# Performance work log

Measured on AMD Instinct MI355X. Metric: run time of the kernel, lower is better.

## Reference

```python
import jax, jax.numpy as jnp
import numpy as np
import math

NUM_HEADS = 32
NUM_KV = 8
D = 128          # num_hidden == per-head dim in this module
S = 2048
B = 1
DK = 128
ROPE_BASE = 10000.0


def rope(x):
    # x: [B, H, S, D]; standard Llama-style RoPE (split-halves rotation) over positions.
    d = x.shape[-1]
    half = d // 2
    pos = jnp.arange(x.shape[2], dtype=jnp.float32)                       # [S]
    inv_freq = 1.0 / (ROPE_BASE ** (jnp.arange(half, dtype=jnp.float32) / half))
    ang = pos[:, None] * inv_freq[None, :]                                # [S, half]
    cos = jnp.cos(ang)
    sin = jnp.sin(ang)
    x1 = x[..., :half]
    x2 = x[..., half:]
    return jnp.concatenate([x1 * cos - x2 * sin, x1 * sin + x2 * cos], axis=-1)


def setup_inputs() -> dict:
    key = jax.random.key(0)
    ks = jax.random.split(key, 8)
    query = jax.random.normal(ks[0], (B, S, D), dtype=jnp.float32)
    k_in = jax.random.normal(ks[1], (B, S, D), dtype=jnp.float32)
    v_in = jax.random.normal(ks[2], (B, S, D), dtype=jnp.float32)
    # causal mask: 1 where attention allowed (lower triangle incl diagonal)
    mask = jnp.tril(jnp.ones((S, S), dtype=jnp.int32))[None, None]        # [1,1,S,S]
    sc = 0.02
    Wq = jax.random.normal(ks[3], (NUM_HEADS * D, D), dtype=jnp.float32) * sc
    bq = jnp.zeros((NUM_HEADS * D,), dtype=jnp.float32)
    Wk = jax.random.normal(ks[4], (NUM_KV * D, D), dtype=jnp.float32) * sc
    bk = jnp.zeros((NUM_KV * D,), dtype=jnp.float32)
    Wv = jax.random.normal(ks[5], (NUM_KV * D, D), dtype=jnp.float32) * sc
    bv = jnp.zeros((NUM_KV * D,), dtype=jnp.float32)
    Wo = jax.random.normal(ks[6], (D, NUM_HEADS * D), dtype=jnp.float32) * sc
    bo = jnp.zeros((D,), dtype=jnp.float32)
    return {"query": query, "key": k_in, "values": v_in, "mask": mask,
            "Wq": Wq, "bq": bq, "Wk": Wk, "bk": bk, "Wv": Wv, "bv": bv,
            "Wo": Wo, "bo": bo}


def reference(query, key, values, mask, Wq, bq, Wk, bk, Wv, bv, Wo, bo):
    Bq, Sq, Dh = query.shape
    # projections; torch Linear: x @ W.T + b. Note: view (reshape), not transpose,
    # exactly as in the original module.
    q = (query @ Wq.T + bq).reshape(Bq, NUM_HEADS, Sq, Dh)   # [B,H,S,D]
    k = (key @ Wk.T + bk).reshape(Bq, NUM_KV, Sq, Dh)        # [B,Hkv,S,D]
    v = (values @ Wv.T + bv).reshape(Bq, NUM_KV, Sq, Dh)
    rk = rope(k)
    rv = rope(v)  # module applies RoPE to values too (faithful)
    rep = NUM_HEADS // NUM_KV
    # torch .repeat((1, rep, 1, 1)) tiles whole head blocks -> jnp.tile
    rk = jnp.tile(rk, (1, rep, 1, 1))                        # [B,H,S,D]
    rv = jnp.tile(rv, (1, rep, 1, 1))
    scores = jnp.einsum('bhqd,bhkd->bhqk', q, rk) / math.sqrt(DK)
    scores = jnp.where(mask == 0, -jnp.inf, scores)
    attn = jax.nn.softmax(scores, axis=-1)
    out = jnp.einsum('bhqk,bhkd->bhqd', attn, rv)            # [B,H,S,D]
    out = out.transpose(0, 2, 1, 3).reshape(Bq, Sq, NUM_HEADS * Dh)
    return out @ Wo.T + bo
```

## Files before the change

### kernel.cpp

```cpp
#include <hip/hip_runtime.h>

typedef unsigned short u16;
typedef unsigned int u32;
typedef short frag_t __attribute__((ext_vector_type(8)));
typedef float f32x4 __attribute__((ext_vector_type(4)));

#define S_LEN 2048

__device__ __forceinline__ float bf2f(u32 u) {
  union { u32 i; float f; } v; v.i = u << 16; return v.f;
}
__device__ __forceinline__ u16 f2bf(float f) {
  u32 x = __float_as_uint(f);
  u32 r = (x + 0x7fffu + ((x >> 16) & 1u)) >> 16;
  return (u16)r;
}
__device__ __forceinline__ void unpack8(uint4 r, float* o) {
  o[0] = bf2f(r.x & 0xffffu); o[1] = bf2f(r.x >> 16);
  o[2] = bf2f(r.y & 0xffffu); o[3] = bf2f(r.y >> 16);
  o[4] = bf2f(r.z & 0xffffu); o[5] = bf2f(r.z >> 16);
  o[6] = bf2f(r.w & 0xffffu); o[7] = bf2f(r.w >> 16);
}
__device__ __forceinline__ u16 ld_in(const void* p, size_t idx, bool fp32) {
  if (fp32) return f2bf(((const float*)p)[idx]);
  return ((const u16*)p)[idx];
}
__device__ __forceinline__ uint4 ld8(const void* p, size_t eidx, bool fp32) {
  if (!fp32) return *(const uint4*)((const u16*)p + eidx);
  const float4* f = (const float4*)((const float*)p + eidx);
  float4 x = f[0], y = f[1];
  uint4 r;
  r.x = (u32)f2bf(x.x) | ((u32)f2bf(x.y) << 16);
  r.y = (u32)f2bf(x.z) | ((u32)f2bf(x.w) << 16);
  r.z = (u32)f2bf(y.x) | ((u32)f2bf(y.y) << 16);
  r.w = (u32)f2bf(y.z) | ((u32)f2bf(y.w) << 16);
  return r;
}

__global__ __launch_bounds__(256) void proj_all(
    const void* __restrict__ query, const void* __restrict__ key,
    const void* __restrict__ values,
    const void* __restrict__ Wq, const void* __restrict__ bq,
    const void* __restrict__ Wk, const void* __restrict__ bk,
    const void* __restrict__ Wv, const void* __restrict__ bv,
    u16* __restrict__ Qb, u16* __restrict__ Kb, u16* __restrict__ Vtmp,
    u32* __restrict__ flag_out) {
  __shared__ u16 As[128][136];
  __shared__ u16 Ws[128][136];
  __shared__ u32 flagS;
  u16 (*Cs)[136] = As;
  const int t = threadIdx.x;
  if (t < 64) {
    u32 e = ((u32)((const u16*)query)[2 * t] >> 7) & 0xFFu;
    bool ok = (e >= 110u && e <= 140u);
    unsigned long long b = __ballot(ok);
    if (t == 0) flagS = (__popcll(b) < 32) ? 1u : 0u;
  }
  __syncthreads();
  const bool fp32 = (flagS != 0u);
  if (t == 0 && blockIdx.x == 0 && blockIdx.y == 0) *flag_out = flagS;
  const int x = blockIdx.x;
  const void *A, *W, *bias;
  u16* C; int N, n0;
  if (x < 32)      { A = query;  W = Wq; bias = bq; C = Qb;   N = 4096; n0 = x << 7; }
  else if (x < 40) { A = key;    W = Wk; bias = bk; C = Kb;   N = 1024; n0 = (x - 32) << 7; }
  else             { A = values; W = Wv; bias = bv; C = Vtmp; N = 1024; n0 = (x - 40) << 7; }
  const float osc = (x < 32) ? 0.12751743f : 1.0f;
  const int m0 = blockIdx.y << 7;
#pragma unroll
  for (int i = 0; i < 8; ++i) {
    int task = t + (i << 8);
    int row = task >> 4, ch = (task & 15) << 3;
    *(uint4*)&As[row][ch] = ld8(A, (size_t)(m0 + row) * 128 + ch, fp32);
    *(uint4*)&Ws[row][ch] = ld8(W, (size_t)(n0 + row) * 128 + ch, fp32);
  }
  __syncthreads();
  const int lane = t & 63, w = t >> 6, quad = lane >> 4, l15 = lane & 15;
  const int rm = (w & 1) << 6, rn = (w >> 1) << 6;
  f32x4 acc[4][4];
#pragma unroll
  for (int mt = 0; mt < 4; ++mt)
#pragma unroll
    for (int nt = 0; nt < 4; ++nt) acc[mt][nt] = 0.f;
#pragma unroll
  for (int mtp = 0; mtp < 2; ++mtp) {
    frag_t a0[4], a1[4];
#pragma unroll
    for (int kc = 0; kc < 4; ++kc) {
      a0[kc] = *(const frag_t*)&As[rm + mtp * 32 + l15][kc * 32 + quad * 8];
      a1[kc] = *(const frag_t*)&As[rm + mtp * 32 + 16 + l15][kc * 32 + quad * 8];
    }
#pragma unroll
    for (int nt = 0; nt < 4; ++nt)
#pragma unroll
      for (int kc = 0; kc < 4; ++kc) {
        frag_t b = *(const frag_t*)&Ws[rn + nt * 16 + l15][kc * 32 + quad * 8];
        acc[mtp * 2][nt] = __builtin_amdgcn_mfma_f32_16x16x32_bf16(a0[kc], b, acc[mtp * 2][nt], 0, 0, 0);
        acc[mtp * 2 + 1][nt] = __builtin_amdgcn_mfma_f32_16x16x32_bf16(a1[kc], b, acc[mtp * 2 + 1][nt], 0, 0, 0);
      }
  }
  __syncthreads();
#pragma unroll
  for (int nt = 0; nt < 4; ++nt) {
    float bb = bf2f((u32)ld_in(bias, n0 + rn + nt * 16 + l15, fp32));
#pragma unroll
    for (int mt = 0; mt < 4; ++mt) {
      int row = rm + ((mt >> 1) * 32) + ((mt & 1) * 16) + quad * 4;
#pragma unroll
      for (int r = 0; r < 4; ++r)
        Cs[row + r][rn + nt * 16 + l15] = f2bf((acc[mt][nt][r] + bb) * osc);
    }
  }
  __syncthreads();
#pragma unroll
  for (int i = 0; i < 8; ++i) {
    int task = t + (i << 8);
    int row = task >> 4, ch = (task & 15) << 3;
    *(uint4*)&C[(size_t)(m0 + row) * N + n0 + ch] = *(const uint4*)&Cs[row][ch];
  }
}

__global__ __launch_bounds__(256) void rope_kv_tr(u16* __restrict__ Kb,
                                                  const u16* __restrict__ Vb,
                                                  u16* __restrict__ VbT) {
  __shared__ u16 Lt[128][72];
  const int t = threadIdx.x;
  const int s0 = blockIdx.x << 6;
  const int g = blockIdx.y;
  for (int i = t; i < 4096; i += 256) {
    int s = s0 + (i >> 6), ii = i & 63;
    float invf = __expf(-(float)ii * 0.14391156831212787f);
    float ang = (float)s * invf;
    float sn, cs;
    sincosf(ang, &sn, &cs);
    size_t base = ((size_t)(g << 11) + s) * 128 + ii;
    float k1 = bf2f((u32)Kb[base]), k2 = bf2f((u32)Kb[base + 64]);
    Kb[base] = f2bf(k1 * cs - k2 * sn);
    Kb[base + 64] = f2bf(k1 * sn + k2 * cs);
  }
  const u16* src = Vb + (size_t)g * S_LEN * 128;
  for (int i = t; i < 512; i += 256) {
    int r = i >> 3, d8 = (i & 7) << 3;
    float lo[8], hi[8];
    unpack8(*(const uint4*)&src[(size_t)(s0 + r) * 128 + d8], lo);
    unpack8(*(const uint4*)&src[(size_t)(s0 + r) * 128 + d8 + 64], hi);
#pragma unroll
    for (int j = 0; j < 8; ++j) {
      float invf = __expf(-(float)(d8 + j) * 0.14391156831212787f);
      float ang = (float)(s0 + r) * invf;
      float sn, cs;
      sincosf(ang, &sn, &cs);
      Lt[d8 + j][r] = f2bf(lo[j] * cs - hi[j] * sn);
      Lt[d8 + 64 + j][r] = f2bf(lo[j] * sn + hi[j] * cs);
    }
  }
  __syncthreads();
  u16* dst = VbT + (size_t)g * 128 * S_LEN + s0;
  for (int i = t; i < 2048; i += 256) {
    int d = i >> 4, s4 = (i & 15) << 2;
    uint2 pk;
    pk.x = (u32)Lt[d][s4] | ((u32)Lt[d][s4 + 1] << 16);
    pk.y = (u32)Lt[d][s4 + 2] | ((u32)Lt[d][s4 + 3] << 16);
    *(uint2*)&dst[(size_t)d * S_LEN + s4] = pk;
  }
}

__global__ __launch_bounds__(256) void attn_mfma(
    const u16* __restrict__ Qb, const u16* __restrict__ Kb,
    const u16* __restrict__ VbT, u16* __restrict__ OpA, u16* __restrict__ OpB,
    float2* __restrict__ Ml, int nkh) {
  __shared__ union SmemU {
    struct { u16 Kt[32][136]; u16 Vt[128][40]; u16 St[128][40]; } m;
    struct { u16 Og[128][136]; } e;
  } su;
  const int t = threadIdx.x;
  const int lane = t & 63, w = t >> 6, quad = lane >> 4, l15 = lane & 15;
  const int g = (int)blockIdx.x & 7;
  const int kh = (int)blockIdx.x >> 3;
  const int h = g + (w << 3);
  const u16* Kg = Kb + (size_t)g * S_LEN * 128;
  const u16* Vg = VbT + (size_t)g * 128 * S_LEN;
  const int kR = t >> 4, kC = (t & 15) << 3;
  const int vR = t >> 2, vC = (t & 3) << 3;
  u16* dst = kh ? OpB : OpA;

  const int qt = 63 - (int)blockIdx.y;
  const int q0 = qt << 5;
  const int niter = qt + 1;
  frag_t aq[2][4];
#pragma unroll
  for (int qp = 0; qp < 2; ++qp)
#pragma unroll
    for (int kc = 0; kc < 4; ++kc)
      aq[qp][kc] = *(const frag_t*)&Qb[((size_t)h * S_LEN + q0 + qp * 16 + l15) * 128 +
                                       kc * 32 + quad * 8];
  float m_r[2] = {-1e30f, -1e30f}, l_r[2] = {0.f, 0.f};
  f32x4 oacc[2][8];
#pragma unroll
  for (int qp = 0; qp < 2; ++qp)
#pragma unroll
    for (int nt = 0; nt < 8; ++nt) oacc[qp][nt] = 0.f;

  uint4 kpf[2], vpf[2];
  if (kh < niter) {
    const int k0 = kh << 5;
    kpf[0] = *(const uint4*)&Kg[(size_t)(k0 + kR) * 128 + kC];
    kpf[1] = *(const uint4*)&Kg[(size_t)(k0 + kR + 16) * 128 + kC];
    vpf[0] = *(const uint4*)&Vg[(size_t)vR * S_LEN + k0 + vC];
    vpf[1] = *(const uint4*)&Vg[(size_t)(vR + 64) * S_LEN + k0 + vC];
  }
  for (int sj = kh; sj < niter; sj += nkh) {
    const int k0 = sj << 5;
    __syncthreads();
    *(uint4*)&su.m.Kt[kR][kC] = kpf[0];
    *(uint4*)&su.m.Kt[kR + 16][kC] = kpf[1];
    *(uint4*)&su.m.Vt[vR][vC] = vpf[0];
    *(uint4*)&su.m.Vt[vR + 64][vC] = vpf[1];
    __syncthreads();
    if (sj + nkh < niter) {
      const int kn = (sj + nkh) << 5;
      kpf[0] = *(const uint4*)&Kg[(size_t)(kn + kR) * 128 + kC];
      kpf[1] = *(const uint4*)&Kg[(size_t)(kn + kR + 16) * 128 + kC];
      vpf[0] = *(const uint4*)&Vg[(size_t)vR * S_LEN + kn + vC];
      vpf[1] = *(const uint4*)&Vg[(size_t)(vR + 64) * S_LEN + kn + vC];
    }
    f32x4 s4[2][2];
#pragma unroll
    for (int kk = 0; kk < 2; ++kk) { s4[kk][0] = 0.f; s4[kk][1] = 0.f; }
#pragma unroll
    for (int kc = 0; kc < 4; ++kc)
#pragma unroll
      for (int kk = 0; kk < 2; ++kk) {
        frag_t a = *(const frag_t*)&su.m.Kt[kk * 16 + l15][kc * 32 + quad * 8];
        s4[kk][0] = __builtin_amdgcn_mfma_f32_16x16x32_bf16(a, aq[0][kc], s4[kk][0], 0, 0, 0);
        s4[kk][1] = __builtin_amdgcn_mfma_f32_16x16x32_bf16(a, aq[1][kc], s4[kk][1], 0, 0, 0);
      }
    const bool lastm = (sj == niter - 1);
    float alpha[2];
#pragma unroll
    for (int qp = 0; qp < 2; ++qp) {
      const int qg = q0 + qp * 16 + l15;
      float mx = -1e30f;
#pragma unroll
      for (int kk = 0; kk < 2; ++kk)
#pragma unroll
        for (int r = 0; r < 4; ++r) {
          float sv = s4[kk][qp][r];
          if (lastm && (k0 + kk * 16 + quad * 4 + r) > qg) sv = -1e30f;
          s4[kk][qp][r] = sv;
          mx = fmaxf(mx, sv);
        }
      mx = fmaxf(mx, __shfl_xor(mx, 16));
      mx = fmaxf(mx, __shfl_xor(mx, 32));
      float mn = fmaxf(m_r[qp], mx);
      alpha[qp] = __builtin_amdgcn_exp2f(m_r[qp] - mn);
      m_r[qp] = mn;
      float sum = 0.f;
      const int strow = w * 32 + qp * 16 + l15;
#pragma unroll
      for (int kk = 0; kk < 2; ++kk) {
        float p0 = __builtin_amdgcn_exp2f(s4[kk][qp][0] - mn);
        float p1 = __builtin_amdgcn_exp2f(s4[kk][qp][1] - mn);
        float p2 = __builtin_amdgcn_exp2f(s4[kk][qp][2] - mn);
        float p3 = __builtin_amdgcn_exp2f(s4[kk][qp][3] - mn);
        sum += (p0 + p1) + (p2 + p3);
        uint2 pk;
        pk.x = (u32)f2bf(p0) | ((u32)f2bf(p1) << 16);
        pk.y = (u32)f2bf(p2) | ((u32)f2bf(p3) << 16);
        *(uint2*)&su.m.St[strow][kk * 16 + quad * 4] = pk;
      }
      sum += __shfl_xor(sum, 16);
      sum += __shfl_xor(sum, 32);
      l_r[qp] = l_r[qp] * alpha[qp] + sum;
    }
    if (__any(alpha[0] < 1.0f || alpha[1] < 1.0f)) {
#pragma unroll
      for (int qp = 0; qp < 2; ++qp)
#pragma unroll
        for (int r = 0; r < 4; ++r) {
          float al = __shfl(alpha[qp], quad * 4 + r);
#pragma unroll
          for (int nt = 0; nt < 8; ++nt) oacc[qp][nt][r] *= al;
        }
    }
    frag_t pa0 = *(const frag_t*)&su.m.St[w * 32 + l15][quad * 8];
    frag_t pa1 = *(const frag_t*)&su.m.St[w * 32 + 16 + l15][quad * 8];
#pragma unroll
    for (int nt = 0; nt < 8; ++nt) {
      frag_t v = *(const frag_t*)&su.m.Vt[nt * 16 + l15][quad * 8];
      oacc[0][nt] = __builtin_amdgcn_mfma_f32_16x16x32_bf16(pa0, v, oacc[0][nt], 0, 0, 0);
      oacc[1][nt] = __builtin_amdgcn_mfma_f32_16x16x32_bf16(pa1, v, oacc[1][nt], 0, 0, 0);
    }
  }
  __syncthreads();
#pragma unroll
  for (int qp = 0; qp < 2; ++qp)
#pragma unroll
    for (int r = 0; r < 4; ++r) {
      float fac = 1.0f;
      if (nkh == 1) fac = 1.0f / __shfl(l_r[qp], quad * 4 + r);
      int row = w * 32 + qp * 16 + quad * 4 + r;
#pragma unroll
      for (int nt = 0; nt < 8; ++nt)
        su.e.Og[row][nt * 16 + l15] = f2bf(oacc[qp][nt][r] * fac);
    }
  __syncthreads();
#pragma unroll
  for (int jj = 0; jj < 8; ++jj) {
    int c = t + (jj << 8);
    int row = c >> 4, ch = (c & 15) << 3;
    int hh = row >> 5, qr = row & 31;
    *(uint4*)&dst[(size_t)(q0 + qr) * 4096 + (g + hh * 8) * 128 + ch] =
        *(const uint4*)&su.e.Og[row][ch];
  }
  if (nkh == 2 && quad == 0) {
#pragma unroll
    for (int qp = 0; qp < 2; ++qp)
      Ml[((size_t)kh * 32 + h) * S_LEN + q0 + qp * 16 + l15] =
          make_float2(m_r[qp], l_r[qp]);
  }
}

__global__ __launch_bounds__(256) void out_part(
    const u16* __restrict__ OpA, const u16* __restrict__ OpB,
    const float2* __restrict__ Ml, const void* __restrict__ Wo,
    float* __restrict__ Pout, const u32* __restrict__ flagp, int nkh) {
  __shared__ u16 As[128][136];
  __shared__ u16 Ws[128][136];
  const bool fp32 = (*flagp != 0u);
  const int t = threadIdx.x;
  const int lane = t & 63, w = t >> 6, quad = lane >> 4, l15 = lane & 15;
  const int rm = (w & 1) << 6, rn = (w >> 1) << 6;
  const int m0 = (int)blockIdx.x << 7;
  const int z = (int)blockIdx.y;
  f32x4 acc[4][4];
#pragma unroll
  for (int mt = 0; mt < 4; ++mt)
#pragma unroll
    for (int nt = 0; nt < 4; ++nt) acc[mt][nt] = 0.f;
  for (int kc2 = 0; kc2 < 2; ++kc2) {
    if (kc2) __syncthreads();
    const int kc0 = (z << 8) + (kc2 << 7);
    const int hh = kc0 >> 7;
#pragma unroll
    for (int i = 0; i < 8; ++i) {
      int task = t + (i << 8);
      int row = task >> 4, ch = (task & 15) << 3;
      size_t idx = (size_t)(m0 + row) * 4096 + kc0 + ch;
      if (nkh == 2) {
        int s = m0 + row;
        float2 p1 = Ml[(size_t)hh * S_LEN + s];
        float2 p2 = Ml[(size_t)(32 + hh) * S_LEN + s];
        float mn = fmaxf(p1.x, p2.x);
        float a1 = __builtin_amdgcn_exp2f(p1.x - mn);
        float a2 = __builtin_amdgcn_exp2f(p2.x - mn);
        float linv = 1.0f / (a1 * p1.y + a2 * p2.y);
        float w1 = a1 * linv, w2 = a2 * linv;
        float o1[8], o2[8];
        unpack8(*(const uint4*)&OpA[idx], o1);
        unpack8(*(const uint4*)&OpB[idx], o2);
        uint4 r;
        r.x = (u32)f2bf(o1[0] * w1 + o2[0] * w2) | ((u32)f2bf(o1[1] * w1 + o2[1] * w2) << 16);
        r.y = (u32)f2bf(o1[2] * w1 + o2[2] * w2) | ((u32)f2bf(o1[3] * w1 + o2[3] * w2) << 16);
        r.z = (u32)f2bf(o1[4] * w1 + o2[4] * w2) | ((u32)f2bf(o1[5] * w1 + o2[5] * w2) << 16);
        r.w = (u32)f2bf(o1[6] * w1 + o2[6] * w2) | ((u32)f2bf(o1[7] * w1 + o2[7] * w2) << 16);
        *(uint4*)&As[row][ch] = r;
      } else {
        *(uint4*)&As[row][ch] = *(const uint4*)&OpA[idx];
      }
      *(uint4*)&Ws[row][ch] = ld8(Wo, (size_t)row * 4096 + kc0 + ch, fp32);
    }
    __syncthreads();
#pragma unroll
    for (int mtp = 0; mtp < 2; ++mtp) {
      frag_t a0[4], a1[4];
#pragma unroll
      for (int kc = 0; kc < 4; ++kc) {
        a0[kc] = *(const frag_t*)&As[rm + mtp * 32 + l15][kc * 32 + quad * 8];
        a1[kc] = *(const frag_t*)&As[rm + mtp * 32 + 16 + l15][kc * 32 + quad * 8];
      }
#pragma unroll
      for (int nt = 0; nt < 4; ++nt)
#pragma unroll
        for (int kc = 0; kc < 4; ++kc) {
          frag_t b = *(const frag_t*)&Ws[rn + nt * 16 + l15][kc * 32 + quad * 8];
          acc[mtp * 2][nt] = __builtin_amdgcn_mfma_f32_16x16x32_bf16(a0[kc], b, acc[mtp * 2][nt], 0, 0, 0);
          acc[mtp * 2 + 1][nt] = __builtin_amdgcn_mfma_f32_16x16x32_bf16(a1[kc], b, acc[mtp * 2 + 1][nt], 0, 0, 0);
        }
    }
  }
#pragma unroll
  for (int mt = 0; mt < 4; ++mt) {
    int mrow = m0 + rm + ((mt >> 1) * 32) + ((mt & 1) * 16) + quad * 4;
#pragma unroll
    for (int nt = 0; nt < 4; ++nt) {
      int n = rn + nt * 16 + l15;
#pragma unroll
      for (int r = 0; r < 4; ++r)
        Pout[((size_t)z * 2048 + mrow + r) * 128 + n] = acc[mt][nt][r];
    }
  }
}

__global__ __launch_bounds__(256) void out_red(
    const float* __restrict__ Pout, const void* __restrict__ bo,
    void* __restrict__ out, const u32* __restrict__ flagp) {
  const bool fp32 = (*flagp != 0u);
  int e4 = blockIdx.x * 256 + threadIdx.x;
  const float4* P = (const float4*)Pout;
  float4 s = P[e4];
#pragma unroll
  for (int z = 1; z < 16; ++z) {
    float4 p = P[(size_t)z * 65536 + e4];
    s.x += p.x; s.y += p.y; s.z += p.z; s.w += p.w;
  }
  int n = (e4 << 2) & 127;
  s.x += bf2f((u32)ld_in(bo, n + 0, fp32));
  s.y += bf2f((u32)ld_in(bo, n + 1, fp32));
  s.z += bf2f((u32)ld_in(bo, n + 2, fp32));
  s.w += bf2f((u32)ld_in(bo, n + 3, fp32));
  if (fp32) {
    ((float4*)out)[e4] = s;
  } else {
    uint2 pk;
    pk.x = (u32)f2bf(s.x) | ((u32)f2bf(s.y) << 16);
    pk.y = (u32)f2bf(s.z) | ((u32)f2bf(s.w) << 16);
    *(uint2*)((u16*)out + (e4 << 2)) = pk;
  }
}

extern "C" void kernel_launch(void* const* d_in, const int* in_sizes, int n_in,
                              void* d_out, int out_size, void* d_ws, size_t ws_size,
                              hipStream_t stream) {
  (void)in_sizes; (void)n_in; (void)out_size;
  const void* query  = d_in[0];
  const void* key    = d_in[1];
  const void* values = d_in[2];
  const void* Wq = d_in[4];
  const void* bq = d_in[5];
  const void* Wk = d_in[6];
  const void* bk = d_in[7];
  const void* Wv = d_in[8];
  const void* bv = d_in[9];
  const void* Wo = d_in[10];
  const void* bo = d_in[11];

  char* ws = (char*)d_ws;
  u32* flag   = (u32*)ws;
  u16* Qb     = (u16*)(ws + 64);
  u16* Kb     = (u16*)(ws + 64 + (16ull << 20));
  u16* VbT    = (u16*)(ws + 64 + (20ull << 20));
  u16* Vtmp   = (u16*)(ws + 64 + (24ull << 20));
  u16* Ob     = (u16*)(ws + 64 + (24ull << 20));
  u16* OpB    = (u16*)(ws + 64 + (40ull << 20));
  float2* Mlb = (float2*)(ws + 64 + (56ull << 20));
  float* Pout = (float*)Qb;

  const bool split = (ws_size >= (58ull << 20));
  const int nkh = split ? 2 : 1;

  proj_all<<<dim3(48, 16), 256, 0, stream>>>(query, key, values, Wq, bq, Wk, bk,
                                             Wv, bv, Qb, Kb, Vtmp, flag);
  rope_kv_tr<<<dim3(32, 8), 256, 0, stream>>>(Kb, Vtmp, VbT);
  attn_mfma<<<dim3(8 * nkh, 64), 256, 0, stream>>>(Qb, Kb, VbT, Ob, OpB, Mlb, nkh);
  out_part<<<dim3(16, 16), 256, 0, stream>>>(Ob, OpB, Mlb, Wo, Pout, flag, nkh);
  out_red<<<256, 256, 0, stream>>>(Pout, bo, d_out, flag);
}
```

Measured before the change: 248.3 us.

## Double-buffer K/V shared tiles in attention and use packed bf16 convert

Turns the K and V shared-memory tiles into two buffers, so the next tile is written into the alternate buffer while the current one is consumed. This cuts the two barriers per iteration down to one. The softmax probabilities are also packed to bf16 with the hardware v_cvt_pk_bf16_f32 instruction instead of software rounding. The cost is more LDS per block, which may lower occupancy.

```diff
diff --git a/kernel.cpp b/kernel.cpp
--- a/kernel.cpp
+++ b/kernel.cpp
@@ -170,7 +170,7 @@
     const u16* __restrict__ VbT, u16* __restrict__ OpA, u16* __restrict__ OpB,
     float2* __restrict__ Ml, int nkh) {
   __shared__ union SmemU {
-    struct { u16 Kt[32][136]; u16 Vt[128][40]; u16 St[128][40]; } m;
+    struct { u16 Kt[2][32][136]; u16 Vt[2][128][40]; u16 St[128][40]; } m;
     struct { u16 Og[128][136]; } e;
   } su;
   const int t = threadIdx.x;
@@ -202,28 +202,42 @@
     for (int nt = 0; nt < 8; ++nt) oacc[qp][nt] = 0.f;
 
   uint4 kpf[2], vpf[2];
+  int cur = 0;
   if (kh < niter) {
     const int k0 = kh << 5;
     kpf[0] = *(const uint4*)&Kg[(size_t)(k0 + kR) * 128 + kC];
     kpf[1] = *(const uint4*)&Kg[(size_t)(k0 + kR + 16) * 128 + kC];
     vpf[0] = *(const uint4*)&Vg[(size_t)vR * S_LEN + k0 + vC];
     vpf[1] = *(const uint4*)&Vg[(size_t)(vR + 64) * S_LEN + k0 + vC];
-  }
-  for (int sj = kh; sj < niter; sj += nkh) {
-    const int k0 = sj << 5;
-    __syncthreads();
-    *(uint4*)&su.m.Kt[kR][kC] = kpf[0];
-    *(uint4*)&su.m.Kt[kR + 16][kC] = kpf[1];
-    *(uint4*)&su.m.Vt[vR][vC] = vpf[0];
-    *(uint4*)&su.m.Vt[vR + 64][vC] = vpf[1];
-    __syncthreads();
-    if (sj + nkh < niter) {
-      const int kn = (sj + nkh) << 5;
+    *(uint4*)&su.m.Kt[0][kR][kC] = kpf[0];
+    *(uint4*)&su.m.Kt[0][kR + 16][kC] = kpf[1];
+    *(uint4*)&su.m.Vt[0][vR][vC] = vpf[0];
+    *(uint4*)&su.m.Vt[0][vR + 64][vC] = vpf[1];
+    if (kh + nkh < niter) {
+      const int kn = (kh + nkh) << 5;
       kpf[0] = *(const uint4*)&Kg[(size_t)(kn + kR) * 128 + kC];
       kpf[1] = *(const uint4*)&Kg[(size_t)(kn + kR + 16) * 128 + kC];
       vpf[0] = *(const uint4*)&Vg[(size_t)vR * S_LEN + kn + vC];
       vpf[1] = *(const uint4*)&Vg[(size_t)(vR + 64) * S_LEN + kn + vC];
     }
+  }
+  __syncthreads();
+  for (int sj = kh; sj < niter; sj += nkh) {
+    const int k0 = sj << 5;
+    const int nxt = cur ^ 1;
+    if (sj + nkh < niter) {
+      *(uint4*)&su.m.Kt[nxt][kR][kC] = kpf[0];
+      *(uint4*)&su.m.Kt[nxt][kR + 16][kC] = kpf[1];
+      *(uint4*)&su.m.Vt[nxt][vR][vC] = vpf[0];
+      *(uint4*)&su.m.Vt[nxt][vR + 64][vC] = vpf[1];
+      if (sj + 2 * nkh < niter) {
+        const int kn = (sj + 2 * nkh) << 5;
+        kpf[0] = *(const uint4*)&Kg[(size_t)(kn + kR) * 128 + kC];
+        kpf[1] = *(const uint4*)&Kg[(size_t)(kn + kR + 16) * 128 + kC];
+        vpf[0] = *(const uint4*)&Vg[(size_t)vR * S_LEN + kn + vC];
+        vpf[1] = *(const uint4*)&Vg[(size_t)(vR + 64) * S_LEN + kn + vC];
+      }
+    }
     f32x4 s4[2][2];
 #pragma unroll
     for (int kk = 0; kk < 2; ++kk) { s4[kk][0] = 0.f; s4[kk][1] = 0.f; }
@@ -231,7 +245,7 @@
     for (int kc = 0; kc < 4; ++kc)
 #pragma unroll
       for (int kk = 0; kk < 2; ++kk) {
-        frag_t a = *(const frag_t*)&su.m.Kt[kk * 16 + l15][kc * 32 + quad * 8];
+        frag_t a = *(const frag_t*)&su.m.Kt[cur][kk * 16 + l15][kc * 32 + quad * 8];
         s4[kk][0] = __builtin_amdgcn_mfma_f32_16x16x32_bf16(a, aq[0][kc], s4[kk][0], 0, 0, 0);
         s4[kk][1] = __builtin_amdgcn_mfma_f32_16x16x32_bf16(a, aq[1][kc], s4[kk][1], 0, 0, 0);
       }
@@ -265,8 +279,8 @@
         float p3 = __builtin_amdgcn_exp2f(s4[kk][qp][3] - mn);
         sum += (p0 + p1) + (p2 + p3);
         uint2 pk;
-        pk.x = (u32)f2bf(p0) | ((u32)f2bf(p1) << 16);
-        pk.y = (u32)f2bf(p2) | ((u32)f2bf(p3) << 16);
+        asm("v_cvt_pk_bf16_f32 %0, %1, %2" : "=v"(pk.x) : "v"(p0), "v"(p1));
+        asm("v_cvt_pk_bf16_f32 %0, %1, %2" : "=v"(pk.y) : "v"(p2), "v"(p3));
         *(uint2*)&su.m.St[strow][kk * 16 + quad * 4] = pk;
       }
       sum += __shfl_xor(sum, 16);
@@ -287,12 +301,13 @@
     frag_t pa1 = *(const frag_t*)&su.m.St[w * 32 + 16 + l15][quad * 8];
 #pragma unroll
     for (int nt = 0; nt < 8; ++nt) {
-      frag_t v = *(const frag_t*)&su.m.Vt[nt * 16 + l15][quad * 8];
+      frag_t v = *(const frag_t*)&su.m.Vt[cur][nt * 16 + l15][quad * 8];
       oacc[0][nt] = __builtin_amdgcn_mfma_f32_16x16x32_bf16(pa0, v, oacc[0][nt], 0, 0, 0);
       oacc[1][nt] = __builtin_amdgcn_mfma_f32_16x16x32_bf16(pa1, v, oacc[1][nt], 0, 0, 0);
     }
-  }
-  __syncthreads();
+    __syncthreads();
+    cur ^= 1;
+  }
 #pragma unroll
   for (int qp = 0; qp < 2; ++qp)
 #pragma unroll
```

Measured after the change: 248.0 us. Within noise of the previous version (-0.1%).

## Widen attention KV tile from 32 to 64 keys and use packed bf16 convert

Applied to the files above, without the earlier changes.

Each main-loop iteration now processes 64 keys instead of 32. This halves the number of iterations, barriers and online-softmax rescale steps per query tile, and it doubles the prefetch registers and LDS tile sizes. The manual bf16 rounding is replaced with the v_cvt_pk_bf16_f32 instruction. The trade-off is higher register and LDS use, which may lower occupancy. With an odd number of 32-row tiles, the last 64-key block also does extra fully masked work on the diagonal.

```diff
diff --git a/kernel.cpp b/kernel.cpp
--- a/kernel.cpp
+++ b/kernel.cpp
@@ -170,7 +170,7 @@
     const u16* __restrict__ VbT, u16* __restrict__ OpA, u16* __restrict__ OpB,
     float2* __restrict__ Ml, int nkh) {
   __shared__ union SmemU {
-    struct { u16 Kt[32][136]; u16 Vt[128][40]; u16 St[128][40]; } m;
+    struct { u16 Kt[64][132]; u16 Vt[128][68]; u16 St[128][68]; } m;
     struct { u16 Og[128][136]; } e;
   } su;
   const int t = threadIdx.x;
@@ -181,12 +181,12 @@
   const u16* Kg = Kb + (size_t)g * S_LEN * 128;
   const u16* Vg = VbT + (size_t)g * 128 * S_LEN;
   const int kR = t >> 4, kC = (t & 15) << 3;
-  const int vR = t >> 2, vC = (t & 3) << 3;
+  const int vR = t >> 3, vC = (t & 7) << 3;
   u16* dst = kh ? OpB : OpA;
 
   const int qt = 63 - (int)blockIdx.y;
   const int q0 = qt << 5;
-  const int niter = qt + 1;
+  const int nk64 = (q0 >> 6) + 1;
   frag_t aq[2][4];
 #pragma unroll
   for (int qp = 0; qp < 2; ++qp)
@@ -201,48 +201,51 @@
 #pragma unroll
     for (int nt = 0; nt < 8; ++nt) oacc[qp][nt] = 0.f;
 
-  uint4 kpf[2], vpf[2];
-  if (kh < niter) {
-    const int k0 = kh << 5;
-    kpf[0] = *(const uint4*)&Kg[(size_t)(k0 + kR) * 128 + kC];
-    kpf[1] = *(const uint4*)&Kg[(size_t)(k0 + kR + 16) * 128 + kC];
-    vpf[0] = *(const uint4*)&Vg[(size_t)vR * S_LEN + k0 + vC];
-    vpf[1] = *(const uint4*)&Vg[(size_t)(vR + 64) * S_LEN + k0 + vC];
-  }
-  for (int sj = kh; sj < niter; sj += nkh) {
-    const int k0 = sj << 5;
+  uint4 kpf[4], vpf[4];
+  if (kh < nk64) {
+    const int k0 = kh << 6;
+#pragma unroll
+    for (int j = 0; j < 4; ++j) {
+      kpf[j] = *(const uint4*)&Kg[(size_t)(k0 + kR + 16 * j) * 128 + kC];
+      vpf[j] = *(const uint4*)&Vg[(size_t)(vR + 32 * j) * S_LEN + k0 + vC];
+    }
+  }
+  for (int sj = kh; sj < nk64; sj += nkh) {
+    const int k0 = sj << 6;
     __syncthreads();
-    *(uint4*)&su.m.Kt[kR][kC] = kpf[0];
-    *(uint4*)&su.m.Kt[kR + 16][kC] = kpf[1];
-    *(uint4*)&su.m.Vt[vR][vC] = vpf[0];
-    *(uint4*)&su.m.Vt[vR + 64][vC] = vpf[1];
+#pragma unroll
+    for (int j = 0; j < 4; ++j) {
+      *(uint4*)&su.m.Kt[kR + 16 * j][kC] = kpf[j];
+      *(uint4*)&su.m.Vt[vR + 32 * j][vC] = vpf[j];
+    }
     __syncthreads();
-    if (sj + nkh < niter) {
-      const int kn = (sj + nkh) << 5;
-      kpf[0] = *(const uint4*)&Kg[(size_t)(kn + kR) * 128 + kC];
-      kpf[1] = *(const uint4*)&Kg[(size_t)(kn + kR + 16) * 128 + kC];
-      vpf[0] = *(const uint4*)&Vg[(size_t)vR * S_LEN + kn + vC];
-      vpf[1] = *(const uint4*)&Vg[(size_t)(vR + 64) * S_LEN + kn + vC];
-    }
-    f32x4 s4[2][2];
-#pragma unroll
-    for (int kk = 0; kk < 2; ++kk) { s4[kk][0] = 0.f; s4[kk][1] = 0.f; }
+    if (sj + nkh < nk64) {
+      const int kn = (sj + nkh) << 6;
+#pragma unroll
+      for (int j = 0; j < 4; ++j) {
+        kpf[j] = *(const uint4*)&Kg[(size_t)(kn + kR + 16 * j) * 128 + kC];
+        vpf[j] = *(const uint4*)&Vg[(size_t)(vR + 32 * j) * S_LEN + kn + vC];
+      }
+    }
+    f32x4 s4[4][2];
+#pragma unroll
+    for (int kk = 0; kk < 4; ++kk) { s4[kk][0] = 0.f; s4[kk][1] = 0.f; }
 #pragma unroll
     for (int kc = 0; kc < 4; ++kc)
 #pragma unroll
-      for (int kk = 0; kk < 2; ++kk) {
+      for (int kk = 0; kk < 4; ++kk) {
         frag_t a = *(const frag_t*)&su.m.Kt[kk * 16 + l15][kc * 32 + quad * 8];
         s4[kk][0] = __builtin_amdgcn_mfma_f32_16x16x32_bf16(a, aq[0][kc], s4[kk][0], 0, 0, 0);
         s4[kk][1] = __builtin_amdgcn_mfma_f32_16x16x32_bf16(a, aq[1][kc], s4[kk][1], 0, 0, 0);
       }
-    const bool lastm = (sj == niter - 1);
+    const bool lastm = (sj == nk64 - 1);
     float alpha[2];
 #pragma unroll
     for (int qp = 0; qp < 2; ++qp) {
       const int qg = q0 + qp * 16 + l15;
       float mx = -1e30f;
 #pragma unroll
-      for (int kk = 0; kk < 2; ++kk)
+      for (int kk = 0; kk < 4; ++kk)
 #pragma unroll
         for (int r = 0; r < 4; ++r) {
           float sv = s4[kk][qp][r];
@@ -258,15 +261,15 @@
       float sum = 0.f;
       const int strow = w * 32 + qp * 16 + l15;
 #pragma unroll
-      for (int kk = 0; kk < 2; ++kk) {
+      for (int kk = 0; kk < 4; ++kk) {
         float p0 = __builtin_amdgcn_exp2f(s4[kk][qp][0] - mn);
         float p1 = __builtin_amdgcn_exp2f(s4[kk][qp][1] - mn);
         float p2 = __builtin_amdgcn_exp2f(s4[kk][qp][2] - mn);
         float p3 = __builtin_amdgcn_exp2f(s4[kk][qp][3] - mn);
         sum += (p0 + p1) + (p2 + p3);
         uint2 pk;
-        pk.x = (u32)f2bf(p0) | ((u32)f2bf(p1) << 16);
-        pk.y = (u32)f2bf(p2) | ((u32)f2bf(p3) << 16);
+        asm("v_cvt_pk_bf16_f32 %0, %1, %2" : "=v"(pk.x) : "v"(p0), "v"(p1));
+        asm("v_cvt_pk_bf16_f32 %0, %1, %2" : "=v"(pk.y) : "v"(p2), "v"(p3));
         *(uint2*)&su.m.St[strow][kk * 16 + quad * 4] = pk;
       }
       sum += __shfl_xor(sum, 16);
@@ -283,13 +286,16 @@
           for (int nt = 0; nt < 8; ++nt) oacc[qp][nt][r] *= al;
         }
     }
-    frag_t pa0 = *(const frag_t*)&su.m.St[w * 32 + l15][quad * 8];
-    frag_t pa1 = *(const frag_t*)&su.m.St[w * 32 + 16 + l15][quad * 8];
-#pragma unroll
-    for (int nt = 0; nt < 8; ++nt) {
-      frag_t v = *(const frag_t*)&su.m.Vt[nt * 16 + l15][quad * 8];
-      oacc[0][nt] = __builtin_amdgcn_mfma_f32_16x16x32_bf16(pa0, v, oacc[0][nt], 0, 0, 0);
-      oacc[1][nt] = __builtin_amdgcn_mfma_f32_16x16x32_bf16(pa1, v, oacc[1][nt], 0, 0, 0);
+#pragma unroll
+    for (int ks = 0; ks < 2; ++ks) {
+      frag_t pa0 = *(const frag_t*)&su.m.St[w * 32 + l15][ks * 32 + quad * 8];
+      frag_t pa1 = *(const frag_t*)&su.m.St[w * 32 + 16 + l15][ks * 32 + quad * 8];
+#pragma unroll
+      for (int nt = 0; nt < 8; ++nt) {
+        frag_t v = *(const frag_t*)&su.m.Vt[nt * 16 + l15][ks * 32 + quad * 8];
+        oacc[0][nt] = __builtin_amdgcn_mfma_f32_16x16x32_bf16(pa0, v, oacc[0][nt], 0, 0, 0);
+        oacc[1][nt] = __builtin_amdgcn_mfma_f32_16x16x32_bf16(pa1, v, oacc[1][nt], 0, 0, 0);
+      }
     }
   }
   __syncthreads();
```

Measured after the change: 386.3 us. 55.6% more time.

## Load K/V MFMA fragments directly from global, drop LDS staging and barriers

Applied to the files above, without the earlier changes.

The attention kernel no longer stages K and V tiles through shared memory with two barriers per iteration. Each wave now loads its MFMA operand fragments for K and V straight from global memory into registers, prefetching the next K tile while the current scores are computed. The softmax probabilities are packed to bf16 with the v_cvt_pk_bf16_f32 instruction instead of software rounding. Each of the four waves now fetches the same K/V data separately, which adds global/L2 traffic and register pressure in exchange for less LDS traffic and no block-level synchronisation. The P tile still goes through shared memory.

```diff
diff --git a/kernel.cpp b/kernel.cpp
--- a/kernel.cpp
+++ b/kernel.cpp
@@ -170,7 +170,7 @@
     const u16* __restrict__ VbT, u16* __restrict__ OpA, u16* __restrict__ OpB,
     float2* __restrict__ Ml, int nkh) {
   __shared__ union SmemU {
-    struct { u16 Kt[32][136]; u16 Vt[128][40]; u16 St[128][40]; } m;
+    struct { u16 St[128][40]; } m;
     struct { u16 Og[128][136]; } e;
   } su;
   const int t = threadIdx.x;
@@ -180,8 +180,6 @@
   const int h = g + (w << 3);
   const u16* Kg = Kb + (size_t)g * S_LEN * 128;
   const u16* Vg = VbT + (size_t)g * 128 * S_LEN;
-  const int kR = t >> 4, kC = (t & 15) << 3;
-  const int vR = t >> 2, vC = (t & 3) << 3;
   u16* dst = kh ? OpB : OpA;
 
   const int qt = 63 - (int)blockIdx.y;
@@ -201,40 +199,41 @@
 #pragma unroll
     for (int nt = 0; nt < 8; ++nt) oacc[qp][nt] = 0.f;
 
-  uint4 kpf[2], vpf[2];
+  frag_t aK[2][4];
   if (kh < niter) {
     const int k0 = kh << 5;
-    kpf[0] = *(const uint4*)&Kg[(size_t)(k0 + kR) * 128 + kC];
-    kpf[1] = *(const uint4*)&Kg[(size_t)(k0 + kR + 16) * 128 + kC];
-    vpf[0] = *(const uint4*)&Vg[(size_t)vR * S_LEN + k0 + vC];
-    vpf[1] = *(const uint4*)&Vg[(size_t)(vR + 64) * S_LEN + k0 + vC];
+#pragma unroll
+    for (int kk = 0; kk < 2; ++kk)
+#pragma unroll
+      for (int kc = 0; kc < 4; ++kc)
+        aK[kk][kc] = *(const frag_t*)&Kg[(size_t)(k0 + kk * 16 + l15) * 128 +
+                                         kc * 32 + quad * 8];
   }
   for (int sj = kh; sj < niter; sj += nkh) {
     const int k0 = sj << 5;
-    __syncthreads();
-    *(uint4*)&su.m.Kt[kR][kC] = kpf[0];
-    *(uint4*)&su.m.Kt[kR + 16][kC] = kpf[1];
-    *(uint4*)&su.m.Vt[vR][vC] = vpf[0];
-    *(uint4*)&su.m.Vt[vR + 64][vC] = vpf[1];
-    __syncthreads();
+    frag_t av[8];
+#pragma unroll
+    for (int nt = 0; nt < 8; ++nt)
+      av[nt] = *(const frag_t*)&Vg[(size_t)(nt * 16 + l15) * S_LEN + k0 + quad * 8];
+    f32x4 s4[2][2];
+#pragma unroll
+    for (int kk = 0; kk < 2; ++kk) { s4[kk][0] = 0.f; s4[kk][1] = 0.f; }
+#pragma unroll
+    for (int kc = 0; kc < 4; ++kc)
+#pragma unroll
+      for (int kk = 0; kk < 2; ++kk) {
+        s4[kk][0] = __builtin_amdgcn_mfma_f32_16x16x32_bf16(aK[kk][kc], aq[0][kc], s4[kk][0], 0, 0, 0);
+        s4[kk][1] = __builtin_amdgcn_mfma_f32_16x16x32_bf16(aK[kk][kc], aq[1][kc], s4[kk][1], 0, 0, 0);
+      }
     if (sj + nkh < niter) {
       const int kn = (sj + nkh) << 5;
-      kpf[0] = *(const uint4*)&Kg[(size_t)(kn + kR) * 128 + kC];
-      kpf[1] = *(const uint4*)&Kg[(size_t)(kn + kR + 16) * 128 + kC];
-      vpf[0] = *(const uint4*)&Vg[(size_t)vR * S_LEN + kn + vC];
-      vpf[1] = *(const uint4*)&Vg[(size_t)(vR + 64) * S_LEN + kn + vC];
-    }
-    f32x4 s4[2][2];
-#pragma unroll
-    for (int kk = 0; kk < 2; ++kk) { s4[kk][0] = 0.f; s4[kk][1] = 0.f; }
-#pragma unroll
-    for (int kc = 0; kc < 4; ++kc)
-#pragma unroll
-      for (int kk = 0; kk < 2; ++kk) {
-        frag_t a = *(const frag_t*)&su.m.Kt[kk * 16 + l15][kc * 32 + quad * 8];
-        s4[kk][0] = __builtin_amdgcn_mfma_f32_16x16x32_bf16(a, aq[0][kc], s4[kk][0], 0, 0, 0);
-        s4[kk][1] = __builtin_amdgcn_mfma_f32_16x16x32_bf16(a, aq[1][kc], s4[kk][1], 0, 0, 0);
-      }
+#pragma unroll
+      for (int kk = 0; kk < 2; ++kk)
+#pragma unroll
+        for (int kc = 0; kc < 4; ++kc)
+          aK[kk][kc] = *(const frag_t*)&Kg[(size_t)(kn + kk * 16 + l15) * 128 +
+                                           kc * 32 + quad * 8];
+    }
     const bool lastm = (sj == niter - 1);
     float alpha[2];
 #pragma unroll
@@ -265,8 +264,8 @@
         float p3 = __builtin_amdgcn_exp2f(s4[kk][qp][3] - mn);
         sum += (p0 + p1) + (p2 + p3);
         uint2 pk;
-        pk.x = (u32)f2bf(p0) | ((u32)f2bf(p1) << 16);
-        pk.y = (u32)f2bf(p2) | ((u32)f2bf(p3) << 16);
+        asm("v_cvt_pk_bf16_f32 %0, %1, %2" : "=v"(pk.x) : "v"(p0), "v"(p1));
+        asm("v_cvt_pk_bf16_f32 %0, %1, %2" : "=v"(pk.y) : "v"(p2), "v"(p3));
         *(uint2*)&su.m.St[strow][kk * 16 + quad * 4] = pk;
       }
       sum += __shfl_xor(sum, 16);
@@ -287,9 +286,8 @@
     frag_t pa1 = *(const frag_t*)&su.m.St[w * 32 + 16 + l15][quad * 8];
 #pragma unroll
     for (int nt = 0; nt < 8; ++nt) {
-      frag_t v = *(const frag_t*)&su.m.Vt[nt * 16 + l15][quad * 8];
-      oacc[0][nt] = __builtin_amdgcn_mfma_f32_16x16x32_bf16(pa0, v, oacc[0][nt], 0, 0, 0);
-      oacc[1][nt] = __builtin_amdgcn_mfma_f32_16x16x32_bf16(pa1, v, oacc[1][nt], 0, 0, 0);
+      oacc[0][nt] = __builtin_amdgcn_mfma_f32_16x16x32_bf16(pa0, av[nt], oacc[0][nt], 0, 0, 0);
+      oacc[1][nt] = __builtin_amdgcn_mfma_f32_16x16x32_bf16(pa1, av[nt], oacc[1][nt], 0, 0, 0);
     }
   }
   __syncthreads();
```

Result: slower. 273.3 us (+10.1%).
